# Kernel optimization log

Measured on AMD Instinct MI355X. Metric: run time of the kernel, lower is better.

Reference implementation:

```python
import jax, jax.numpy as jnp
import numpy as np

PI = jnp.pi

def phasor_encode(x):
    # map phase in [-1,1] to unit complex phasor exp(i*pi*x)
    return jnp.exp(jnp.complex64(1j) * PI * x.astype(jnp.float32))

def phasor_act(z):
    # angle of complex activation, normalized back to [-1,1]
    return jnp.angle(z) / PI

def multi_dense(x, w, b):
    # PhasorMultiDense: x [b,t,d], w [h,d,D], b [h,D] (complex bias, ones init)
    xz = phasor_encode(x)                                      # [b,t,d] complex64
    wz = w.astype(jnp.complex64)
    bz = b.astype(jnp.complex64)
    yz = jnp.einsum('btd,hdD->bhtD', xz, wz) + bz[None, :, None, :]
    return phasor_act(yz)                                      # [b,h,t,D] real

def attend(q, k, v):
    # VSA phasor attention: similarity = Re(qz . conj(kz)) / d, softmax, complex bundle of v phasors
    d = q.shape[-1]
    qz = phasor_encode(q)
    kz = phasor_encode(k)
    scores = jnp.real(jnp.einsum('bhtd,bhTd->bhtT', qz, jnp.conj(kz))) / d
    probs = jax.nn.softmax(scores, axis=-1)
    vz = phasor_encode(v)
    out = jnp.einsum('bhtT,bhTd->bhtd', probs.astype(jnp.complex64), vz)
    return phasor_act(out)                                     # [b,h,t,D]

def setup_inputs() -> dict:
    key = jax.random.key(0)
    ks = jax.random.split(key, 8)
    B, Tq, Tkv, D, H = 2, 1024, 1024, 512, 8
    sw = 1.0 / np.sqrt(D)       # VarianceScaling(1.0) fan_in
    swo = 1.0 / np.sqrt(H * D)
    return {
        'query': jax.random.uniform(ks[0], (B, Tq, D), jnp.float32, -1.0, 1.0),
        'keyvalue': jax.random.uniform(ks[1], (B, Tkv, D), jnp.float32, -1.0, 1.0),
        'wq': jax.random.normal(ks[2], (H, D, D), jnp.float32) * sw,
        'bq': jnp.ones((H, D), jnp.float32),
        'wk': jax.random.normal(ks[3], (H, D, D), jnp.float32) * sw,
        'bk': jnp.ones((H, D), jnp.float32),
        'wv': jax.random.normal(ks[4], (H, D, D), jnp.float32) * sw,
        'bv': jnp.ones((H, D), jnp.float32),
        'wo': jax.random.normal(ks[5], (H * D, D), jnp.float32) * swo,
        'bo': jnp.ones((D,), jnp.float32),
    }

def reference(query, keyvalue, wq, bq, wk, bk, wv, bv, wo, bo):
    q = multi_dense(query, wq, bq)        # [b,h,t,D]
    k = multi_dense(keyvalue, wk, bk)
    v = multi_dense(keyvalue, wv, bv)
    r = attend(q, k, v)                   # [b,h,t,D]
    b_, h_, t_, d_ = r.shape
    r_flat = jnp.transpose(r, (0, 2, 1, 3)).reshape(b_, t_, h_ * d_)  # b t (h d)
    # final PhasorDense
    xz = phasor_encode(r_flat)
    z = jnp.einsum('btd,dD->btD', xz, wo.astype(jnp.complex64)) + bo.astype(jnp.complex64)
    return phasor_act(z)                  # [b, t_q, output_channels]
```

## Files before the change

kernel.cpp:

```cpp
#include <hip/hip_runtime.h>
#include <math.h>


#define PI_F 3.14159274101257324f

typedef __attribute__((ext_vector_type(8))) _Float16 half8;
typedef __attribute__((ext_vector_type(4))) _Float16 half4;
typedef __attribute__((ext_vector_type(2))) _Float16 half2v;
typedef __attribute__((ext_vector_type(16))) float f32x16;
typedef unsigned int u32;

#define MFMA32(a, b, c) __builtin_amdgcn_mfma_f32_32x32x16_f16((a), (b), (c), 0, 0, 0)
#define ROWOF(r, ln) (((r) & 3) + 8 * ((r) >> 2) + 4 * ((ln) >> 5))

__device__ __forceinline__ void gll16(const void* g, void* l) {
    __builtin_amdgcn_global_load_lds(
        (const __attribute__((address_space(1))) u32*)g,
        (__attribute__((address_space(3))) u32*)l, 16, 0, 0);
}

__device__ __forceinline__ void split2(float x, _Float16& h, _Float16& l) {
    _Float16 hh = (_Float16)x;
    h = hh;
    l = (_Float16)((x - (float)hh) * 4096.0f);
}

__device__ __forceinline__ size_t feo(int m, int k, int Kd16) {
    return ((size_t)((m >> 5) * Kd16 + (k >> 4))) * 512
           + ((m & 31) + 32 * ((k >> 3) & 1)) * 8 + (k & 7);
}

__device__ __forceinline__ int xcdswz(int bid, int nwg) {
    const int cpx = nwg >> 3;
    return (bid & 7) * cpx + (bid >> 3);
}

__global__ __launch_bounds__(256) void encode_phasor(
    const float* __restrict__ x,
    _Float16* __restrict__ ch, _Float16* __restrict__ cl,
    _Float16* __restrict__ sh, _Float16* __restrict__ sl)
{
    const int idx = blockIdx.x * 256 + threadIdx.x;
    const int m = idx >> 7, k4 = (idx & 127) * 4;
    float4 v = ((const float4*)x)[idx];
    float cc[4], ss[4];
    sincosf(PI_F * v.x, &ss[0], &cc[0]);
    sincosf(PI_F * v.y, &ss[1], &cc[1]);
    sincosf(PI_F * v.z, &ss[2], &cc[2]);
    sincosf(PI_F * v.w, &ss[3], &cc[3]);
    half4 chv, clv, shv, slv;
#pragma unroll
    for (int q = 0; q < 4; ++q) {
        _Float16 a, b;
        split2(cc[q], a, b); chv[q] = a; clv[q] = b;
        split2(ss[q], a, b); shv[q] = a; slv[q] = b;
    }
    const size_t off = feo(m, k4, 32);
    *(half4*)(ch + off) = chv;
    *(half4*)(cl + off) = clv;
    *(half4*)(sh + off) = shv;
    *(half4*)(sl + off) = slv;
}

__global__ __launch_bounds__(256) void tsplit64(
    const float* __restrict__ w, _Float16* __restrict__ th, _Float16* __restrict__ tl,
    int K, int N)
{
    const int kt = blockIdx.x, ntile = blockIdx.y, h = blockIdx.z;
    const int k0 = kt * 64, n0 = ntile * 64;
    __shared__ float T[64][65];
    const int tid = threadIdx.x;
    const float* wb = w + (size_t)h * K * N;
    {
        const int r = tid >> 4, c4 = (tid & 15) * 4;
#pragma unroll
        for (int rr = 0; rr < 64; rr += 16) {
            float4 v = *(const float4*)&wb[(size_t)(k0 + rr + r) * N + n0 + c4];
            T[rr + r][c4 + 0] = v.x; T[rr + r][c4 + 1] = v.y;
            T[rr + r][c4 + 2] = v.z; T[rr + r][c4 + 3] = v.w;
        }
    }
    __syncthreads();
    {
        const int n = n0 + (tid >> 2), kq = k0 + (tid & 3) * 16;
        half8 hv[2], lv[2];
#pragma unroll
        for (int q = 0; q < 16; ++q) {
            float f = T[kq - k0 + q][n - n0];
            _Float16 hh, ll; split2(f, hh, ll);
            hv[q >> 3][q & 7] = hh; lv[q >> 3][q & 7] = ll;
        }
        const size_t hb = (size_t)h * 512 * K;
        const size_t offA = hb + ((size_t)((n >> 5) * (K >> 4) + (kq >> 4))) * 512
                            + (n & 31) * 8;
        *(half8*)(th + offA) = hv[0]; *(half8*)(th + offA + 256) = hv[1];
        *(half8*)(tl + offA) = lv[0]; *(half8*)(tl + offA + 256) = lv[1];
    }
}

template<bool VT>
__global__ __launch_bounds__(256, 2) void proj_mfma(
    const _Float16* __restrict__ xch, const _Float16* __restrict__ xcl,
    const _Float16* __restrict__ xsh, const _Float16* __restrict__ xsl,
    const _Float16* __restrict__ wth, const _Float16* __restrict__ wtl,
    const float* __restrict__ bias,
    _Float16* __restrict__ ozh, _Float16* __restrict__ ozl,
    _Float16* __restrict__ vc_h, _Float16* __restrict__ vc_l,
    _Float16* __restrict__ vs_h, _Float16* __restrict__ vs_l,
    int h0, int hcnt)
{
    const int m0 = blockIdx.x * 64;
    const int hc = blockIdx.y >> 2;
    const int n0 = (blockIdx.y & 3) * 128;
    __shared__ char lds[32768];
    const int tid = threadIdx.x, wv = tid >> 6, ln = tid & 63;
    const int wr = wv >> 1, wc = wv & 1, lm32 = ln & 31;

    const size_t abase = ((size_t)((m0 >> 5) + wr)) * 32 * 512 + ln * 8;
    const _Float16* pxc[2] = { xch + abase, xcl + abase };
    const _Float16* pxs[2] = { xsh + abase, xsl + abase };

    const char* spB[4]; int dpB[4];
#pragma unroll
    for (int u = 0; u < 4; ++u) {
        const int g = wv * 4 + u;
        const int jt = g >> 2, hl = (g >> 1) & 1, ks = g & 1;
        const _Float16* base = (hl ? wtl : wth) + (size_t)hc * 262144;
        spB[u] = (const char*)(base
                 + ((size_t)(((n0 + jt * 32) >> 5) * 32 + ks)) * 512 + ln * 8);
        dpB[u] = g * 1024;
    }

    f32x16 ach[2] = {}, acl[2] = {}, ash[2] = {}, asl[2] = {};

    auto LOADA = [&](int s, half8 (&ac)[2][2], half8 (&as)[2][2]) {
#pragma unroll
        for (int hl = 0; hl < 2; ++hl)
#pragma unroll
            for (int ks = 0; ks < 2; ++ks) {
                ac[hl][ks] = *(const half8*)(pxc[hl] + (2 * s + ks) * 512);
                as[hl][ks] = *(const half8*)(pxs[hl] + (2 * s + ks) * 512);
            }
    };
    auto STAGEB = [&](int s, int buf) {
#pragma unroll
        for (int u = 0; u < 4; ++u)
            gll16(spB[u] + (size_t)s * 2048, lds + buf + dpB[u]);
    };
    auto MSTEP = [&](int buf, half8 (&ac)[2][2], half8 (&as)[2][2]) {
        half8 w0[2][2], w1[2][2];
#pragma unroll
        for (int ks = 0; ks < 2; ++ks)
#pragma unroll
            for (int j = 0; j < 2; ++j) {
                const int gb = (wc * 2 + j) * 4 + ks;
                w0[ks][j] = *(const half8*)(lds + buf + gb * 1024 + ln * 16);
                w1[ks][j] = *(const half8*)(lds + buf + (gb + 2) * 1024 + ln * 16);
            }
        __builtin_amdgcn_s_setprio(1);
#pragma unroll
        for (int ks = 0; ks < 2; ++ks)
#pragma unroll
            for (int j = 0; j < 2; ++j) {
                ach[j] = MFMA32(ac[0][ks], w0[ks][j], ach[j]);
                acl[j] = MFMA32(ac[0][ks], w1[ks][j], acl[j]);
                acl[j] = MFMA32(ac[1][ks], w0[ks][j], acl[j]);
                ash[j] = MFMA32(as[0][ks], w0[ks][j], ash[j]);
                asl[j] = MFMA32(as[0][ks], w1[ks][j], asl[j]);
                asl[j] = MFMA32(as[1][ks], w0[ks][j], asl[j]);
            }
        __builtin_amdgcn_s_setprio(0);
    };

    half8 Ac0[2][2], As0[2][2], Ac1[2][2], As1[2][2];
    LOADA(0, Ac0, As0); STAGEB(0, 0);
    const int NS = 16;
    for (int s = 0; s < NS; s += 2) {
        __syncthreads();
        STAGEB(s + 1, 16384); LOADA(s + 1, Ac1, As1);
        MSTEP(0, Ac0, As0);
        __syncthreads();
        if (s + 2 < NS) { STAGEB(s + 2, 0); LOADA(s + 2, Ac0, As0); }
        MSTEP(16384, Ac1, As1);
    }

    const float LS = 1.0f / 4096.0f;
    const int b = m0 >> 10, tbase = m0 & 1023;
    const size_t zz = (size_t)(b * hcnt + hc);
    if constexpr (!VT) {
        const size_t zb = zz << 20;
#pragma unroll
        for (int j = 0; j < 2; ++j) {
            const int nloc = wc * 64 + j * 32 + lm32;
            const float bval = bias[(size_t)(h0 + hc) * 512 + n0 + nloc];
            const int kk = 2 * (n0 + nloc);
#pragma unroll
            for (int r = 0; r < 16; ++r) {
                const int mloc = wr * 32 + ROWOF(r, ln);
                float yc = ach[j][r] + acl[j][r] * LS + bval;
                float ys = ash[j][r] + asl[j][r] * LS;
                float inv = 1.0f / sqrtf(fmaxf(yc * yc + ys * ys, 1e-36f));
                float c = yc * inv, sn = ys * inv;
                _Float16 chh, chl, shh, shl;
                split2(c, chh, chl); split2(sn, shh, shl);
                const size_t off = zb + feo(tbase + mloc, kk, 64);
                half2v hv, lv;
                hv[0] = chh; hv[1] = shh; lv[0] = chl; lv[1] = shl;
                *(half2v*)(ozh + off) = hv;
                *(half2v*)(ozl + off) = lv;
            }
        }
    } else {
        _Float16 vh[4][2][16];
#pragma unroll
        for (int j = 0; j < 2; ++j) {
            const int nloc = wc * 64 + j * 32 + lm32;
            const float bval = bias[(size_t)(h0 + hc) * 512 + n0 + nloc];
#pragma unroll
            for (int r = 0; r < 16; ++r) {
                float yc = ach[j][r] + acl[j][r] * LS + bval;
                float ys = ash[j][r] + asl[j][r] * LS;
                float inv = 1.0f / sqrtf(fmaxf(yc * yc + ys * ys, 1e-36f));
                _Float16 a, bq_;
                split2(yc * inv, a, bq_); vh[0][j][r] = a; vh[1][j][r] = bq_;
                split2(ys * inv, a, bq_); vh[2][j][r] = a; vh[3][j][r] = bq_;
            }
        }
        const size_t zvb = zz * 524288;
        _Float16* outp[4] = { vc_h, vc_l, vs_h, vs_l };
#pragma unroll
        for (int p = 0; p < 4; ++p) {
            __syncthreads();
            _Float16* T = (_Float16*)lds;
#pragma unroll
            for (int j = 0; j < 2; ++j) {
                const int dloc = wc * 64 + j * 32 + lm32;
#pragma unroll
                for (int r = 0; r < 16; ++r)
                    T[dloc * 72 + wr * 32 + ROWOF(r, ln)] = vh[p][j][r];
            }
            __syncthreads();
            const int d_l = tid >> 1, seg = tid & 1;
            const int dg = n0 + d_l;
#pragma unroll
            for (int q = 0; q < 4; ++q) {
                const int tg = tbase + seg * 32 + q * 8;
                const size_t off = zvb + feo(dg, tg, 64);
                *(half8*)(outp[p] + off) = *(const half8*)(T + d_l * 72 + seg * 32 + q * 8);
            }
        }
    }
}

__global__ __launch_bounds__(256, 2) void scores_mfma(
    const _Float16* __restrict__ qzh, const _Float16* __restrict__ qzl,
    const _Float16* __restrict__ kzh, const _Float16* __restrict__ kzl,
    float* __restrict__ S, int Z)
{
    const int wg = xcdswz(blockIdx.x, Z * 64);
    const int z = wg >> 6;
    const int rem = wg & 63;
    const int m0 = (rem & 7) << 7, n0 = (rem >> 3) << 7;
    __shared__ char lds[32768];
    const size_t zb = (size_t)z << 20;
    const int tid = threadIdx.x, wv = tid >> 6, ln = tid & 63;
    const int wr = wv >> 1, wc = wv & 1, lm32 = ln & 31;

    const _Float16* pa[2] = { qzh + zb + ln * 8, qzl + zb + ln * 8 };
    const char* spB[4]; int dpB[4];
#pragma unroll
    for (int u = 0; u < 4; ++u) {
        const int g = wv * 4 + u;
        const int jt = g >> 2, hl = (g >> 1) & 1, ks = g & 1;
        spB[u] = (const char*)((hl ? kzl : kzh) + zb
                 + ((size_t)(((n0 + jt * 32) >> 5) * 64 + ks)) * 512 + ln * 8);
        dpB[u] = g * 1024;
    }

    f32x16 acch[2][2] = {}, accl[2][2] = {};

    auto LOADA = [&](int s, half8 (&a)[2][2][2]) {
#pragma unroll
        for (int hl = 0; hl < 2; ++hl)
#pragma unroll
            for (int i = 0; i < 2; ++i)
#pragma unroll
                for (int ks = 0; ks < 2; ++ks)
                    a[hl][i][ks] = *(const half8*)(pa[hl]
                        + ((size_t)((m0 >> 5) + wr * 2 + i) * 64 + 2 * s + ks) * 512);
    };
    auto STAGEB = [&](int s, int buf) {
#pragma unroll
        for (int u = 0; u < 4; ++u)
            gll16(spB[u] + (size_t)s * 2048, lds + buf + dpB[u]);
    };
    auto MSTEP = [&](int buf, half8 (&a)[2][2][2]) {
        half8 bh[2][2], bl[2][2];
#pragma unroll
        for (int ks = 0; ks < 2; ++ks)
#pragma unroll
            for (int j = 0; j < 2; ++j) {
                const int gb = (wc * 2 + j) * 4 + ks;
                bh[ks][j] = *(const half8*)(lds + buf + gb * 1024 + ln * 16);
                bl[ks][j] = *(const half8*)(lds + buf + (gb + 2) * 1024 + ln * 16);
            }
        __builtin_amdgcn_s_setprio(1);
#pragma unroll
        for (int ks = 0; ks < 2; ++ks)
#pragma unroll
            for (int i = 0; i < 2; ++i)
#pragma unroll
                for (int j = 0; j < 2; ++j) {
                    acch[i][j] = MFMA32(a[0][i][ks], bh[ks][j], acch[i][j]);
                    accl[i][j] = MFMA32(a[0][i][ks], bl[ks][j], accl[i][j]);
                    accl[i][j] = MFMA32(a[1][i][ks], bh[ks][j], accl[i][j]);
                }
        __builtin_amdgcn_s_setprio(0);
    };

    half8 A0[2][2][2], A1[2][2][2];
    LOADA(0, A0); STAGEB(0, 0);
    const int NS = 32;
    for (int s = 0; s < NS; s += 2) {
        __syncthreads();
        STAGEB(s + 1, 16384); LOADA(s + 1, A1);
        MSTEP(0, A0);
        __syncthreads();
        if (s + 2 < NS) { STAGEB(s + 2, 0); LOADA(s + 2, A0); }
        MSTEP(16384, A1);
    }
    const float LS = 1.0f / 4096.0f, SC = 1.0f / 512.0f;
#pragma unroll
    for (int i = 0; i < 2; ++i)
#pragma unroll
        for (int j = 0; j < 2; ++j)
#pragma unroll
            for (int r = 0; r < 16; ++r) {
                const int row = m0 + wr * 64 + i * 32 + ROWOF(r, ln);
                const int col = n0 + wc * 64 + j * 32 + lm32;
                S[zb + (size_t)row * 1024 + col] =
                    (acch[i][j][r] + accl[i][j][r] * LS) * SC;
            }
}

__global__ __launch_bounds__(256) void softmax_split(
    const float* __restrict__ S, _Float16* __restrict__ Ph, _Float16* __restrict__ Pl)
{
    const int z = blockIdx.x >> 10, t = blockIdx.x & 1023;
    const float* p = S + ((size_t)blockIdx.x << 10);
    const int tid = threadIdx.x;
    float4 v = ((const float4*)p)[tid];
    float m = fmaxf(fmaxf(v.x, v.y), fmaxf(v.z, v.w));
#pragma unroll
    for (int off = 32; off >= 1; off >>= 1)
        m = fmaxf(m, __shfl_xor(m, off));
    __shared__ float redm[4], reds[4];
    const int wid = tid >> 6, lane = tid & 63;
    if (lane == 0) redm[wid] = m;
    __syncthreads();
    m = fmaxf(fmaxf(redm[0], redm[1]), fmaxf(redm[2], redm[3]));
    float4 e;
    e.x = expf(v.x - m); e.y = expf(v.y - m);
    e.z = expf(v.z - m); e.w = expf(v.w - m);
    float s = (e.x + e.y) + (e.z + e.w);
#pragma unroll
    for (int off = 32; off >= 1; off >>= 1)
        s += __shfl_xor(s, off);
    if (lane == 0) reds[wid] = s;
    __syncthreads();
    s = (reds[0] + reds[1]) + (reds[2] + reds[3]);
    e.x /= s; e.y /= s; e.z /= s; e.w /= s;
    half4 hv, lv;
    _Float16 a, b;
    split2(e.x, a, b); hv[0] = a; lv[0] = b;
    split2(e.y, a, b); hv[1] = a; lv[1] = b;
    split2(e.z, a, b); hv[2] = a; lv[2] = b;
    split2(e.w, a, b); hv[3] = a; lv[3] = b;
    const size_t off = ((size_t)z << 20) + feo(t, tid * 4, 64);
    *(half4*)(Ph + off) = hv;
    *(half4*)(Pl + off) = lv;
}

__global__ __launch_bounds__(256, 2) void pv_mfma(
    const _Float16* __restrict__ Ph, const _Float16* __restrict__ Pl,
    const _Float16* __restrict__ vch, const _Float16* __restrict__ vcl,
    const _Float16* __restrict__ vsh, const _Float16* __restrict__ vsl,
    _Float16* __restrict__ rch, _Float16* __restrict__ rcl,
    _Float16* __restrict__ rsh, _Float16* __restrict__ rsl,
    int h0, int hcnt, int Z)
{
    const int wg = xcdswz(blockIdx.x, Z * 64);
    const int z = wg >> 6;
    const int rem = wg & 63;
    const int m0 = (rem & 7) << 7, n0 = (rem >> 3) << 6;
    __shared__ char lds[32768];
    const int tid = threadIdx.x, wv = tid >> 6, ln = tid & 63;
    const int wr = wv >> 1, wc = wv & 1, lm32 = ln & 31;

    const size_t zb = (size_t)z << 20, zvb = (size_t)z * 524288;
    const _Float16* pa[2] = { Ph + zb + ln * 8, Pl + zb + ln * 8 };
    const char* spB[4]; int dpB[4];
#pragma unroll
    for (int u = 0; u < 4; ++u) {
        const int g = wv * 4 + u;
        const int pl = g >> 3, dt = (g >> 2) & 1, hl = (g >> 1) & 1, ks = g & 1;
        const _Float16* base = pl ? (hl ? vsl : vsh) : (hl ? vcl : vch);
        spB[u] = (const char*)(base + zvb
                 + ((size_t)(((n0 + dt * 32) >> 5) * 64 + ks)) * 512 + ln * 8);
        dpB[u] = g * 1024;
    }

    f32x16 ac_h[2] = {}, ac_l[2] = {}, as_h[2] = {}, as_l[2] = {};

    auto LOADA = [&](int s, half8 (&a)[2][2][2]) {
#pragma unroll
        for (int hl = 0; hl < 2; ++hl)
#pragma unroll
            for (int i = 0; i < 2; ++i)
#pragma unroll
                for (int ks = 0; ks < 2; ++ks)
                    a[hl][i][ks] = *(const half8*)(pa[hl]
                        + ((size_t)((m0 >> 5) + wr * 2 + i) * 64 + 2 * s + ks) * 512);
    };
    auto STAGEB = [&](int s, int buf) {
#pragma unroll
        for (int u = 0; u < 4; ++u)
            gll16(spB[u] + (size_t)s * 2048, lds + buf + dpB[u]);
    };
    auto MSTEP = [&](int buf, half8 (&a)[2][2][2]) {
        half8 vc[2][2], vs[2][2];
#pragma unroll
        for (int hl = 0; hl < 2; ++hl)
#pragma unroll
            for (int ks = 0; ks < 2; ++ks) {
                vc[hl][ks] = *(const half8*)(lds + buf + (wc * 4 + hl * 2 + ks) * 1024 + ln * 16);
                vs[hl][ks] = *(const half8*)(lds + buf + (8 + wc * 4 + hl * 2 + ks) * 1024 + ln * 16);
            }
        __builtin_amdgcn_s_setprio(1);
#pragma unroll
        for (int ks = 0; ks < 2; ++ks)
#pragma unroll
            for (int i = 0; i < 2; ++i) {
                ac_h[i] = MFMA32(a[0][i][ks], vc[0][ks], ac_h[i]);
                ac_l[i] = MFMA32(a[0][i][ks], vc[1][ks], ac_l[i]);
                ac_l[i] = MFMA32(a[1][i][ks], vc[0][ks], ac_l[i]);
                as_h[i] = MFMA32(a[0][i][ks], vs[0][ks], as_h[i]);
                as_l[i] = MFMA32(a[0][i][ks], vs[1][ks], as_l[i]);
                as_l[i] = MFMA32(a[1][i][ks], vs[0][ks], as_l[i]);
            }
        __builtin_amdgcn_s_setprio(0);
    };

    half8 A0[2][2][2], A1[2][2][2];
    LOADA(0, A0); STAGEB(0, 0);
    const int NS = 32;
    for (int s = 0; s < NS; s += 2) {
        __syncthreads();
        STAGEB(s + 1, 16384); LOADA(s + 1, A1);
        MSTEP(0, A0);
        __syncthreads();
        if (s + 2 < NS) { STAGEB(s + 2, 0); LOADA(s + 2, A0); }
        MSTEP(16384, A1);
    }
    const float LS = 1.0f / 4096.0f;
    const int b = z / hcnt, hg = h0 + z % hcnt;
#pragma unroll
    for (int i = 0; i < 2; ++i)
#pragma unroll
        for (int r = 0; r < 16; ++r) {
            const int t = m0 + wr * 64 + i * 32 + ROWOF(r, ln);
            const int d = n0 + wc * 32 + lm32;
            float zc = ac_h[i][r] + ac_l[i][r] * LS;
            float zs = as_h[i][r] + as_l[i][r] * LS;
            float inv = 1.0f / sqrtf(fmaxf(zc * zc + zs * zs, 1e-36f));
            _Float16 chh, chl, shh, shl;
            split2(zc * inv, chh, chl);
            split2(zs * inv, shh, shl);
            const size_t off = feo(b * 1024 + t, hg * 512 + d, 256);
            rch[off] = chh; rcl[off] = chl; rsh[off] = shh; rsl[off] = shl;
        }
}

__global__ __launch_bounds__(256, 2) void final_mfma(
    const _Float16* __restrict__ rch, const _Float16* __restrict__ rcl,
    const _Float16* __restrict__ rsh, const _Float16* __restrict__ rsl,
    const _Float16* __restrict__ woh, const _Float16* __restrict__ wol,
    float* __restrict__ pbuf)
{
    const int m0 = blockIdx.x * 64, n0 = blockIdx.y * 128;
    const int kspl = blockIdx.z;
    const int kf = kspl * 64;
    __shared__ char lds[32768];
    const int tid = threadIdx.x, wv = tid >> 6, ln = tid & 63;
    const int wr = wv >> 1, wc = wv & 1, lm32 = ln & 31;

    const size_t abase = ((size_t)((m0 >> 5) + wr) * 256 + kf) * 512 + ln * 8;
    const _Float16* prc[2] = { rch + abase, rcl + abase };
    const _Float16* prs[2] = { rsh + abase, rsl + abase };
    const char* spB[4]; int dpB[4];
#pragma unroll
    for (int u = 0; u < 4; ++u) {
        const int g = wv * 4 + u;
        const int jt = g >> 2, hl = (g >> 1) & 1, ks = g & 1;
        spB[u] = (const char*)((hl ? wol : woh)
                 + ((size_t)(((n0 + jt * 32) >> 5) * 256 + kf + ks)) * 512 + ln * 8);
        dpB[u] = g * 1024;
    }

    f32x16 rr_h[2] = {}, rr_l[2] = {}, ri_h[2] = {}, ri_l[2] = {};

    auto LOADA = [&](int s, half8 (&ac)[2][2], half8 (&as)[2][2]) {
#pragma unroll
        for (int hl = 0; hl < 2; ++hl)
#pragma unroll
            for (int ks = 0; ks < 2; ++ks) {
                ac[hl][ks] = *(const half8*)(prc[hl] + (2 * s + ks) * 512);
                as[hl][ks] = *(const half8*)(prs[hl] + (2 * s + ks) * 512);
            }
    };
    auto STAGEB = [&](int s, int buf) {
#pragma unroll
        for (int u = 0; u < 4; ++u)
            gll16(spB[u] + (size_t)s * 2048, lds + buf + dpB[u]);
    };
    auto MSTEP = [&](int buf, half8 (&ac)[2][2], half8 (&as)[2][2]) {
        half8 w0[2][2], w1[2][2];
#pragma unroll
        for (int ks = 0; ks < 2; ++ks)
#pragma unroll
            for (int j = 0; j < 2; ++j) {
                const int gb = (wc * 2 + j) * 4 + ks;
                w0[ks][j] = *(const half8*)(lds + buf + gb * 1024 + ln * 16);
                w1[ks][j] = *(const half8*)(lds + buf + (gb + 2) * 1024 + ln * 16);
            }
        __builtin_amdgcn_s_setprio(1);
#pragma unroll
        for (int ks = 0; ks < 2; ++ks)
#pragma unroll
            for (int j = 0; j < 2; ++j) {
                rr_h[j] = MFMA32(ac[0][ks], w0[ks][j], rr_h[j]);
                rr_l[j] = MFMA32(ac[0][ks], w1[ks][j], rr_l[j]);
                rr_l[j] = MFMA32(ac[1][ks], w0[ks][j], rr_l[j]);
                ri_h[j] = MFMA32(as[0][ks], w0[ks][j], ri_h[j]);
                ri_l[j] = MFMA32(as[0][ks], w1[ks][j], ri_l[j]);
                ri_l[j] = MFMA32(as[1][ks], w0[ks][j], ri_l[j]);
            }
        __builtin_amdgcn_s_setprio(0);
    };

    half8 Ac0[2][2], As0[2][2], Ac1[2][2], As1[2][2];
    LOADA(0, Ac0, As0); STAGEB(0, 0);
    const int NS = 32;
    for (int s = 0; s < NS; s += 2) {
        __syncthreads();
        STAGEB(s + 1, 16384); LOADA(s + 1, Ac1, As1);
        MSTEP(0, Ac0, As0);
        __syncthreads();
        if (s + 2 < NS) { STAGEB(s + 2, 0); LOADA(s + 2, Ac0, As0); }
        MSTEP(16384, Ac1, As1);
    }
    const float LS = 1.0f / 4096.0f;
#pragma unroll
    for (int j = 0; j < 2; ++j) {
        const int ng = n0 + wc * 64 + j * 32 + lm32;
#pragma unroll
        for (int r = 0; r < 16; ++r) {
            const int mg = m0 + wr * 32 + ROWOF(r, ln);
            float2 v;
            v.x = rr_h[j][r] + rr_l[j][r] * LS;
            v.y = ri_h[j][r] + ri_l[j][r] * LS;
            *(float2*)&pbuf[((size_t)(kspl * 2048 + mg) * 512 + ng) * 2] = v;
        }
    }
}

__global__ __launch_bounds__(256) void final_combine(
    const float* __restrict__ pbuf, const float* __restrict__ bo,
    float* __restrict__ out, int KS)
{
    const int m = blockIdx.x, t = threadIdx.x;
    float4 acc = {0.f, 0.f, 0.f, 0.f};
    for (int s = 0; s < KS; ++s) {
        float4 v = *(const float4*)&pbuf[(size_t)(s * 2048 + m) * 1024 + t * 4];
        acc.x += v.x; acc.y += v.y; acc.z += v.z; acc.w += v.w;
    }
    const int n0 = t * 2;
    out[(size_t)m * 512 + n0]     = atan2f(acc.y, acc.x + bo[n0]) / PI_F;
    out[(size_t)m * 512 + n0 + 1] = atan2f(acc.w, acc.z + bo[n0 + 1]) / PI_F;
}

extern "C" void kernel_launch(void* const* d_in, const int* in_sizes, int n_in,
                              void* d_out, int out_size, void* d_ws, size_t ws_size,
                              hipStream_t stream)
{
    (void)in_sizes; (void)n_in; (void)out_size;
    const float* query    = (const float*)d_in[0];
    const float* keyvalue = (const float*)d_in[1];
    const float* wq = (const float*)d_in[2];
    const float* bq = (const float*)d_in[3];
    const float* wk = (const float*)d_in[4];
    const float* bk = (const float*)d_in[5];
    const float* wv = (const float*)d_in[6];
    const float* bv = (const float*)d_in[7];
    const float* wo = (const float*)d_in[8];
    const float* bo = (const float*)d_in[9];
    float* out = (float*)d_out;

    int hcnt;
    if (ws_size >= (size_t)320 * 1024 * 1024) hcnt = 8;
    else if (ws_size >= (size_t)240 * 1024 * 1024) hcnt = 4;
    else hcnt = 2;
    const int Z = 2 * hcnt;
    const int KS = (hcnt == 2) ? 2 : 4;

    char* p = (char*)d_ws;
    auto alloc = [&](size_t bytes) {
        char* r = p;
        p += (bytes + 255) & ~(size_t)255;
        return r;
    };
    const size_t PLX = (size_t)2048 * 512;
    _Float16* xq[4]; for (int i = 0; i < 4; ++i) xq[i] = (_Float16*)alloc(PLX * 2);
    _Float16* xk[4]; for (int i = 0; i < 4; ++i) xk[i] = (_Float16*)alloc(PLX * 2);
    _Float16* woT[2]; for (int i = 0; i < 2; ++i) woT[i] = (_Float16*)alloc((size_t)512 * 4096 * 2);
    const size_t WTE = (size_t)hcnt * 512 * 512;
    _Float16* wqT[2]; for (int i = 0; i < 2; ++i) wqT[i] = (_Float16*)alloc(WTE * 2);
    _Float16* wkT[2]; for (int i = 0; i < 2; ++i) wkT[i] = (_Float16*)alloc(WTE * 2);
    _Float16* wvT[2]; for (int i = 0; i < 2; ++i) wvT[i] = (_Float16*)alloc(WTE * 2);
    const size_t QZE = (size_t)Z * 1024 * 1024;
    _Float16* qz[2]; for (int i = 0; i < 2; ++i) qz[i] = (_Float16*)alloc(QZE * 2);
    _Float16* kz[2]; for (int i = 0; i < 2; ++i) kz[i] = (_Float16*)alloc(QZE * 2);
    float* S = (float*)alloc(QZE * 4);
    const size_t VTE = (size_t)Z * 512 * 1024;
    _Float16* vT[4]; for (int i = 0; i < 4; ++i) vT[i] = (_Float16*)alloc(VTE * 2);
    const size_t RCE = (size_t)2048 * 4096;
    _Float16* rcs[4];
    if (hcnt == 8) {
        for (int i = 0; i < 4; ++i) rcs[i] = (_Float16*)((char*)qz[0] + (size_t)i * RCE * 2);
    } else {
        for (int i = 0; i < 4; ++i) rcs[i] = (_Float16*)alloc(RCE * 2);
    }
    _Float16* Ph = kz[0];
    _Float16* Pl = kz[1];
    float* pbuf = (float*)kz[0];

    dim3 blk(256);

    encode_phasor<<<1024, blk, 0, stream>>>(query, xq[0], xq[1], xq[2], xq[3]);
    encode_phasor<<<1024, blk, 0, stream>>>(keyvalue, xk[0], xk[1], xk[2], xk[3]);
    tsplit64<<<dim3(64, 8, 1), blk, 0, stream>>>(wo, woT[0], woT[1], 4096, 512);

    for (int c = 0; c < 8 / hcnt; ++c) {
        const int h0 = c * hcnt;
        const float* wqc = wq + (size_t)h0 * 512 * 512;
        const float* wkc = wk + (size_t)h0 * 512 * 512;
        const float* wvc = wv + (size_t)h0 * 512 * 512;
        tsplit64<<<dim3(8, 8, hcnt), blk, 0, stream>>>(wqc, wqT[0], wqT[1], 512, 512);
        tsplit64<<<dim3(8, 8, hcnt), blk, 0, stream>>>(wkc, wkT[0], wkT[1], 512, 512);
        tsplit64<<<dim3(8, 8, hcnt), blk, 0, stream>>>(wvc, wvT[0], wvT[1], 512, 512);

        proj_mfma<false><<<dim3(32, hcnt * 4), blk, 0, stream>>>(
            xq[0], xq[1], xq[2], xq[3], wqT[0], wqT[1], bq,
            qz[0], qz[1], nullptr, nullptr, nullptr, nullptr, h0, hcnt);
        proj_mfma<false><<<dim3(32, hcnt * 4), blk, 0, stream>>>(
            xk[0], xk[1], xk[2], xk[3], wkT[0], wkT[1], bk,
            kz[0], kz[1], nullptr, nullptr, nullptr, nullptr, h0, hcnt);
        proj_mfma<true><<<dim3(32, hcnt * 4), blk, 0, stream>>>(
            xk[0], xk[1], xk[2], xk[3], wvT[0], wvT[1], bv,
            nullptr, nullptr, vT[0], vT[1], vT[2], vT[3], h0, hcnt);

        scores_mfma<<<dim3(Z * 64), blk, 0, stream>>>(qz[0], qz[1], kz[0], kz[1], S, Z);
        softmax_split<<<dim3(Z * 1024), blk, 0, stream>>>(S, Ph, Pl);
        pv_mfma<<<dim3(Z * 64), blk, 0, stream>>>(
            Ph, Pl, vT[0], vT[1], vT[2], vT[3],
            rcs[0], rcs[1], rcs[2], rcs[3], h0, hcnt, Z);
    }

    final_mfma<<<dim3(32, 4, KS), blk, 0, stream>>>(
        rcs[0], rcs[1], rcs[2], rcs[3], woT[0], woT[1], pbuf);
    final_combine<<<dim3(2048), blk, 0, stream>>>(pbuf, bo, out, KS);
}
```

Baseline: 595.4 us.

## Stage fragment-layout outputs through LDS and merge encode/split/projection launches

Epilogues in encode, projection, softmax and PV kernels now stage results in LDS and write full 16-byte fragment-layout chunks, replacing scattered 2-byte and 4-byte global stores. Encode, weight-split and Q/K projection launches are merged into fewer kernels via grid z-dimension selection. Softmax is restructured to process 32 rows per block and drops the max subtraction, since scores are bounded by 1 in magnitude. These changes aim to cut store-transaction overhead and launch count, at the cost of extra LDS round trips and barriers.

```diff
diff --git a/kernel.cpp b/kernel.cpp
--- a/kernel.cpp
+++ b/kernel.cpp
@@ -25,41 +25,64 @@
     l = (_Float16)((x - (float)hh) * 4096.0f);
 }
 
-__device__ __forceinline__ size_t feo(int m, int k, int Kd16) {
-    return ((size_t)((m >> 5) * Kd16 + (k >> 4))) * 512
-           + ((m & 31) + 32 * ((k >> 3) & 1)) * 8 + (k & 7);
-}
-
 __device__ __forceinline__ int xcdswz(int bid, int nwg) {
     const int cpx = nwg >> 3;
     return (bid & 7) * cpx + (bid >> 3);
 }
 
 __global__ __launch_bounds__(256) void encode_phasor(
-    const float* __restrict__ x,
-    _Float16* __restrict__ ch, _Float16* __restrict__ cl,
-    _Float16* __restrict__ sh, _Float16* __restrict__ sl)
-{
-    const int idx = blockIdx.x * 256 + threadIdx.x;
-    const int m = idx >> 7, k4 = (idx & 127) * 4;
-    float4 v = ((const float4*)x)[idx];
-    float cc[4], ss[4];
-    sincosf(PI_F * v.x, &ss[0], &cc[0]);
-    sincosf(PI_F * v.y, &ss[1], &cc[1]);
-    sincosf(PI_F * v.z, &ss[2], &cc[2]);
-    sincosf(PI_F * v.w, &ss[3], &cc[3]);
-    half4 chv, clv, shv, slv;
-#pragma unroll
-    for (int q = 0; q < 4; ++q) {
-        _Float16 a, b;
-        split2(cc[q], a, b); chv[q] = a; clv[q] = b;
-        split2(ss[q], a, b); shv[q] = a; slv[q] = b;
-    }
-    const size_t off = feo(m, k4, 32);
-    *(half4*)(ch + off) = chv;
-    *(half4*)(cl + off) = clv;
-    *(half4*)(sh + off) = shv;
-    *(half4*)(sl + off) = slv;
+    const float* __restrict__ xq, const float* __restrict__ xkv,
+    _Float16* __restrict__ qch, _Float16* __restrict__ qcl,
+    _Float16* __restrict__ qsh, _Float16* __restrict__ qsl,
+    _Float16* __restrict__ kch, _Float16* __restrict__ kcl,
+    _Float16* __restrict__ ksh, _Float16* __restrict__ ksl)
+{
+    const int mt = blockIdx.x, yh = blockIdx.y, zi = blockIdx.z;
+    const float* x = zi ? xkv : xq;
+    __shared__ char fb[32768];
+    const int tid = threadIdx.x;
+    const int row = tid >> 3, lc = tid & 7;
+    const float* xr = x + (size_t)(mt * 32 + row) * 512 + yh * 256;
+    for (int c = 0; c < 2; ++c) {
+        if (c) __syncthreads();
+        half8 hs[4][2];
+#pragma unroll
+        for (int g = 0; g < 2; ++g)
+#pragma unroll
+            for (int q = 0; q < 2; ++q) {
+                float4 v = *(const float4*)(xr + c * 128 + lc * 16 + g * 8 + q * 4);
+                float cc[4], ss[4];
+                sincosf(PI_F * v.x, &ss[0], &cc[0]);
+                sincosf(PI_F * v.y, &ss[1], &cc[1]);
+                sincosf(PI_F * v.z, &ss[2], &cc[2]);
+                sincosf(PI_F * v.w, &ss[3], &cc[3]);
+#pragma unroll
+                for (int e = 0; e < 4; ++e) {
+                    _Float16 a, b;
+                    split2(cc[e], a, b); hs[0][g][q * 4 + e] = a; hs[1][g][q * 4 + e] = b;
+                    split2(ss[e], a, b); hs[2][g][q * 4 + e] = a; hs[3][g][q * 4 + e] = b;
+                }
+            }
+#pragma unroll
+        for (int p = 0; p < 4; ++p) {
+            char* base = fb + p * 8192 + lc * 1024 + row * 16;
+            *(half8*)(base) = hs[p][0];
+            *(half8*)(base + 512) = hs[p][1];
+        }
+        __syncthreads();
+#pragma unroll
+        for (int w = 0; w < 8; ++w) {
+            const int u = w * 256 + tid;
+            const int p = u >> 9, rest = u & 511;
+            const int f = rest >> 6, within = rest & 63;
+            _Float16* op;
+            if (zi) op = (p == 0) ? kch : (p == 1) ? kcl : (p == 2) ? ksh : ksl;
+            else    op = (p == 0) ? qch : (p == 1) ? qcl : (p == 2) ? qsh : qsl;
+            const size_t fragG = (size_t)mt * 32 + yh * 16 + c * 8 + f;
+            *(half8*)(op + fragG * 512 + within * 8) =
+                *(const half8*)(fb + p * 8192 + f * 1024 + within * 16);
+        }
+    }
 }
 
 __global__ __launch_bounds__(256) void tsplit64(
@@ -98,17 +121,71 @@
     }
 }
 
-template<bool VT>
-__global__ __launch_bounds__(256, 2) void proj_mfma(
-    const _Float16* __restrict__ xch, const _Float16* __restrict__ xcl,
-    const _Float16* __restrict__ xsh, const _Float16* __restrict__ xsl,
-    const _Float16* __restrict__ wth, const _Float16* __restrict__ wtl,
-    const float* __restrict__ bias,
-    _Float16* __restrict__ ozh, _Float16* __restrict__ ozl,
-    _Float16* __restrict__ vc_h, _Float16* __restrict__ vc_l,
-    _Float16* __restrict__ vs_h, _Float16* __restrict__ vs_l,
+__global__ __launch_bounds__(256) void tsplit_qkv(
+    const float* __restrict__ wq, const float* __restrict__ wk,
+    const float* __restrict__ wv,
+    _Float16* __restrict__ qh, _Float16* __restrict__ ql,
+    _Float16* __restrict__ kh, _Float16* __restrict__ kl,
+    _Float16* __restrict__ vh, _Float16* __restrict__ vl, int hcnt)
+{
+    const int tsel = blockIdx.z / hcnt, h = blockIdx.z % hcnt;
+    const int kt = blockIdx.x, ntile = blockIdx.y;
+    const int k0 = kt * 64, n0 = ntile * 64;
+    const float* w = (tsel == 0) ? wq : (tsel == 1) ? wk : wv;
+    _Float16* th = (tsel == 0) ? qh : (tsel == 1) ? kh : vh;
+    _Float16* tl = (tsel == 0) ? ql : (tsel == 1) ? kl : vl;
+    __shared__ float T[64][65];
+    const int tid = threadIdx.x;
+    const float* wb = w + (size_t)h * 262144;
+    {
+        const int r = tid >> 4, c4 = (tid & 15) * 4;
+#pragma unroll
+        for (int rr = 0; rr < 64; rr += 16) {
+            float4 v = *(const float4*)&wb[(size_t)(k0 + rr + r) * 512 + n0 + c4];
+            T[rr + r][c4 + 0] = v.x; T[rr + r][c4 + 1] = v.y;
+            T[rr + r][c4 + 2] = v.z; T[rr + r][c4 + 3] = v.w;
+        }
+    }
+    __syncthreads();
+    {
+        const int n = n0 + (tid >> 2), kq = k0 + (tid & 3) * 16;
+        half8 hv[2], lv[2];
+#pragma unroll
+        for (int q = 0; q < 16; ++q) {
+            float f = T[kq - k0 + q][n - n0];
+            _Float16 hh, ll; split2(f, hh, ll);
+            hv[q >> 3][q & 7] = hh; lv[q >> 3][q & 7] = ll;
+        }
+        const size_t hb = (size_t)h * 262144;
+        const size_t offA = hb + ((size_t)((n >> 5) * 32 + (kq >> 4))) * 512 + (n & 31) * 8;
+        *(half8*)(th + offA) = hv[0]; *(half8*)(th + offA + 256) = hv[1];
+        *(half8*)(tl + offA) = lv[0]; *(half8*)(tl + offA + 256) = lv[1];
+    }
+}
+
+__global__ __launch_bounds__(256, 2) void proj_qk(
+    const _Float16* __restrict__ qch, const _Float16* __restrict__ qcl,
+    const _Float16* __restrict__ qsh, const _Float16* __restrict__ qsl,
+    const _Float16* __restrict__ kch, const _Float16* __restrict__ kcl,
+    const _Float16* __restrict__ ksh, const _Float16* __restrict__ ksl,
+    const _Float16* __restrict__ wqh, const _Float16* __restrict__ wql,
+    const _Float16* __restrict__ wkh, const _Float16* __restrict__ wkl,
+    const float* __restrict__ bq, const float* __restrict__ bk,
+    _Float16* __restrict__ qzh, _Float16* __restrict__ qzl,
+    _Float16* __restrict__ kzh, _Float16* __restrict__ kzl,
     int h0, int hcnt)
 {
+    const int inp = blockIdx.z;
+    const _Float16* xch = inp ? kch : qch;
+    const _Float16* xcl = inp ? kcl : qcl;
+    const _Float16* xsh = inp ? ksh : qsh;
+    const _Float16* xsl = inp ? ksl : qsl;
+    const _Float16* wth = inp ? wkh : wqh;
+    const _Float16* wtl = inp ? wkl : wql;
+    const float* bias = inp ? bk : bq;
+    _Float16* ozh = inp ? kzh : qzh;
+    _Float16* ozl = inp ? kzl : qzl;
+
     const int m0 = blockIdx.x * 64;
     const int hc = blockIdx.y >> 2;
     const int n0 = (blockIdx.y & 3) * 128;
@@ -187,67 +264,165 @@
     const float LS = 1.0f / 4096.0f;
     const int b = m0 >> 10, tbase = m0 & 1023;
     const size_t zz = (size_t)(b * hcnt + hc);
-    if constexpr (!VT) {
-        const size_t zb = zz << 20;
+    const size_t zb = zz << 20;
+    __syncthreads();
+#pragma unroll
+    for (int p = 0; p < 2; ++p) {
+        if (p) __syncthreads();
 #pragma unroll
         for (int j = 0; j < 2; ++j) {
             const int nloc = wc * 64 + j * 32 + lm32;
             const float bval = bias[(size_t)(h0 + hc) * 512 + n0 + nloc];
-            const int kk = 2 * (n0 + nloc);
+            const int kk = 2 * nloc;
 #pragma unroll
             for (int r = 0; r < 16; ++r) {
                 const int mloc = wr * 32 + ROWOF(r, ln);
                 float yc = ach[j][r] + acl[j][r] * LS + bval;
                 float ys = ash[j][r] + asl[j][r] * LS;
                 float inv = 1.0f / sqrtf(fmaxf(yc * yc + ys * ys, 1e-36f));
-                float c = yc * inv, sn = ys * inv;
-                _Float16 chh, chl, shh, shl;
-                split2(c, chh, chl); split2(sn, shh, shl);
-                const size_t off = zb + feo(tbase + mloc, kk, 64);
-                half2v hv, lv;
-                hv[0] = chh; hv[1] = shh; lv[0] = chl; lv[1] = shl;
-                *(half2v*)(ozh + off) = hv;
-                *(half2v*)(ozl + off) = lv;
-            }
-        }
-    } else {
-        _Float16 vh[4][2][16];
+                _Float16 c_h, c_l, s_h, s_l;
+                split2(yc * inv, c_h, c_l);
+                split2(ys * inv, s_h, s_l);
+                half2v pr;
+                pr[0] = p ? c_l : c_h;
+                pr[1] = p ? s_l : s_h;
+                *(half2v*)(lds + ((mloc >> 5) * 16 + (kk >> 4)) * 1024
+                    + (mloc & 31) * 16 + 512 * ((kk >> 3) & 1) + (kk & 7) * 2) = pr;
+            }
+        }
+        __syncthreads();
+        _Float16* op = p ? ozl : ozh;
+#pragma unroll
+        for (int w = 0; w < 8; ++w) {
+            const int u = w * 256 + tid;
+            const int f = u >> 6, within = u & 63;
+            const int ms = f >> 4, kf = f & 15;
+            *(half8*)(op + zb + (((size_t)(tbase >> 5) + ms) * 64 + (n0 >> 3) + kf) * 512
+                      + within * 8) = *(const half8*)(lds + f * 1024 + within * 16);
+        }
+    }
+}
+
+__global__ __launch_bounds__(256, 2) void proj_v(
+    const _Float16* __restrict__ xch, const _Float16* __restrict__ xcl,
+    const _Float16* __restrict__ xsh, const _Float16* __restrict__ xsl,
+    const _Float16* __restrict__ wth, const _Float16* __restrict__ wtl,
+    const float* __restrict__ bias,
+    _Float16* __restrict__ vc_h, _Float16* __restrict__ vc_l,
+    _Float16* __restrict__ vs_h, _Float16* __restrict__ vs_l,
+    int h0, int hcnt)
+{
+    const int m0 = blockIdx.x * 64;
+    const int hc = blockIdx.y >> 2;
+    const int n0 = (blockIdx.y & 3) * 128;
+    __shared__ char lds[32768];
+    const int tid = threadIdx.x, wv = tid >> 6, ln = tid & 63;
+    const int wr = wv >> 1, wc = wv & 1, lm32 = ln & 31;
+
+    const size_t abase = ((size_t)((m0 >> 5) + wr)) * 32 * 512 + ln * 8;
+    const _Float16* pxc[2] = { xch + abase, xcl + abase };
+    const _Float16* pxs[2] = { xsh + abase, xsl + abase };
+
+    const char* spB[4]; int dpB[4];
+#pragma unroll
+    for (int u = 0; u < 4; ++u) {
+        const int g = wv * 4 + u;
+        const int jt = g >> 2, hl = (g >> 1) & 1, ks = g & 1;
+        const _Float16* base = (hl ? wtl : wth) + (size_t)hc * 262144;
+        spB[u] = (const char*)(base
+                 + ((size_t)(((n0 + jt * 32) >> 5) * 32 + ks)) * 512 + ln * 8);
+        dpB[u] = g * 1024;
+    }
+
+    f32x16 ach[2] = {}, acl[2] = {}, ash[2] = {}, asl[2] = {};
+
+    auto LOADA = [&](int s, half8 (&ac)[2][2], half8 (&as)[2][2]) {
+#pragma unroll
+        for (int hl = 0; hl < 2; ++hl)
+#pragma unroll
+            for (int ks = 0; ks < 2; ++ks) {
+                ac[hl][ks] = *(const half8*)(pxc[hl] + (2 * s + ks) * 512);
+                as[hl][ks] = *(const half8*)(pxs[hl] + (2 * s + ks) * 512);
+            }
+    };
+    auto STAGEB = [&](int s, int buf) {
+#pragma unroll
+        for (int u = 0; u < 4; ++u)
+            gll16(spB[u] + (size_t)s * 2048, lds + buf + dpB[u]);
+    };
+    auto MSTEP = [&](int buf, half8 (&ac)[2][2], half8 (&as)[2][2]) {
+        half8 w0[2][2], w1[2][2];
+#pragma unroll
+        for (int ks = 0; ks < 2; ++ks)
+#pragma unroll
+            for (int j = 0; j < 2; ++j) {
+                const int gb = (wc * 2 + j) * 4 + ks;
+                w0[ks][j] = *(const half8*)(lds + buf + gb * 1024 + ln * 16);
+                w1[ks][j] = *(const half8*)(lds + buf + (gb + 2) * 1024 + ln * 16);
+            }
+        __builtin_amdgcn_s_setprio(1);
+#pragma unroll
+        for (int ks = 0; ks < 2; ++ks)
+#pragma unroll
+            for (int j = 0; j < 2; ++j) {
+                ach[j] = MFMA32(ac[0][ks], w0[ks][j], ach[j]);
+                acl[j] = MFMA32(ac[0][ks], w1[ks][j], acl[j]);
+                acl[j] = MFMA32(ac[1][ks], w0[ks][j], acl[j]);
+                ash[j] = MFMA32(as[0][ks], w0[ks][j], ash[j]);
+                asl[j] = MFMA32(as[0][ks], w1[ks][j], asl[j]);
+                asl[j] = MFMA32(as[1][ks], w0[ks][j], asl[j]);
+            }
+        __builtin_amdgcn_s_setprio(0);
+    };
+
+    half8 Ac0[2][2], As0[2][2], Ac1[2][2], As1[2][2];
+    LOADA(0, Ac0, As0); STAGEB(0, 0);
+    const int NS = 16;
+    for (int s = 0; s < NS; s += 2) {
+        __syncthreads();
+        STAGEB(s + 1, 16384); LOADA(s + 1, Ac1, As1);
+        MSTEP(0, Ac0, As0);
+        __syncthreads();
+        if (s + 2 < NS) { STAGEB(s + 2, 0); LOADA(s + 2, Ac0, As0); }
+        MSTEP(16384, Ac1, As1);
+    }
+
+    const float LS = 1.0f / 4096.0f;
+    const int b = m0 >> 10, tbase = m0 & 1023;
+    const size_t zz = (size_t)(b * hcnt + hc);
+    const size_t zvb = zz * 524288;
+    _Float16* T = (_Float16*)lds;
+#pragma unroll
+    for (int p = 0; p < 4; ++p) {
+        __syncthreads();
 #pragma unroll
         for (int j = 0; j < 2; ++j) {
-            const int nloc = wc * 64 + j * 32 + lm32;
-            const float bval = bias[(size_t)(h0 + hc) * 512 + n0 + nloc];
+            const int dloc = wc * 64 + j * 32 + lm32;
+            const float bval = bias[(size_t)(h0 + hc) * 512 + n0 + dloc];
 #pragma unroll
             for (int r = 0; r < 16; ++r) {
+                const int tloc = wr * 32 + ROWOF(r, ln);
                 float yc = ach[j][r] + acl[j][r] * LS + bval;
                 float ys = ash[j][r] + asl[j][r] * LS;
                 float inv = 1.0f / sqrtf(fmaxf(yc * yc + ys * ys, 1e-36f));
-                _Float16 a, bq_;
-                split2(yc * inv, a, bq_); vh[0][j][r] = a; vh[1][j][r] = bq_;
-                split2(ys * inv, a, bq_); vh[2][j][r] = a; vh[3][j][r] = bq_;
-            }
-        }
-        const size_t zvb = zz * 524288;
-        _Float16* outp[4] = { vc_h, vc_l, vs_h, vs_l };
-#pragma unroll
-        for (int p = 0; p < 4; ++p) {
-            __syncthreads();
-            _Float16* T = (_Float16*)lds;
-#pragma unroll
-            for (int j = 0; j < 2; ++j) {
-                const int dloc = wc * 64 + j * 32 + lm32;
-#pragma unroll
-                for (int r = 0; r < 16; ++r)
-                    T[dloc * 72 + wr * 32 + ROWOF(r, ln)] = vh[p][j][r];
-            }
-            __syncthreads();
-            const int d_l = tid >> 1, seg = tid & 1;
-            const int dg = n0 + d_l;
-#pragma unroll
-            for (int q = 0; q < 4; ++q) {
-                const int tg = tbase + seg * 32 + q * 8;
-                const size_t off = zvb + feo(dg, tg, 64);
-                *(half8*)(outp[p] + off) = *(const half8*)(T + d_l * 72 + seg * 32 + q * 8);
-            }
+                _Float16 hh, ll;
+                if (p < 2) split2(yc * inv, hh, ll);
+                else       split2(ys * inv, hh, ll);
+                T[dloc * 80 + tloc] = (p & 1) ? ll : hh;
+            }
+        }
+        __syncthreads();
+        _Float16* op = (p == 0) ? vc_h : (p == 1) ? vc_l : (p == 2) ? vs_h : vs_l;
+#pragma unroll
+        for (int w = 0; w < 4; ++w) {
+            const int u = w * 256 + tid;
+            const int f = u >> 6, within = u & 63;
+            const int ds_ = f >> 2, tf = f & 3;
+            const int d = ds_ * 32 + (within & 31);
+            const int tl = tf * 16 + (within >> 5) * 8;
+            half8 vv = *(const half8*)(T + d * 80 + tl);
+            *(half8*)(op + zvb + (((size_t)((n0 >> 5) + ds_)) * 64 + (tbase >> 4) + tf) * 512
+                      + within * 8) = vv;
         }
     }
 }
@@ -343,42 +518,52 @@
             }
 }
 
-__global__ __launch_bounds__(256) void softmax_split(
+__global__ __launch_bounds__(256) void softmax_frag(
     const float* __restrict__ S, _Float16* __restrict__ Ph, _Float16* __restrict__ Pl)
 {
-    const int z = blockIdx.x >> 10, t = blockIdx.x & 1023;
-    const float* p = S + ((size_t)blockIdx.x << 10);
+    const int z = blockIdx.x >> 5, tt = blockIdx.x & 31;
+    const float* Sb = S + ((size_t)z << 20) + ((size_t)tt << 15);
     const int tid = threadIdx.x;
-    float4 v = ((const float4*)p)[tid];
-    float m = fmaxf(fmaxf(v.x, v.y), fmaxf(v.z, v.w));
-#pragma unroll
-    for (int off = 32; off >= 1; off >>= 1)
-        m = fmaxf(m, __shfl_xor(m, off));
-    __shared__ float redm[4], reds[4];
-    const int wid = tid >> 6, lane = tid & 63;
-    if (lane == 0) redm[wid] = m;
+    const int row = tid >> 3, lc = tid & 7;
+    __shared__ float rsum[32];
+    __shared__ char fb[32768];
+    const float* prow = Sb + (size_t)row * 1024 + lc * 128;
+    float s = 0.f;
+    for (int q = 0; q < 32; ++q) {
+        float4 v = *(const float4*)(prow + q * 4);
+        s += (expf(v.x) + expf(v.y)) + (expf(v.z) + expf(v.w));
+    }
+    s += __shfl_xor(s, 1); s += __shfl_xor(s, 2); s += __shfl_xor(s, 4);
+    if (lc == 0) rsum[row] = s;
     __syncthreads();
-    m = fmaxf(fmaxf(redm[0], redm[1]), fmaxf(redm[2], redm[3]));
-    float4 e;
-    e.x = expf(v.x - m); e.y = expf(v.y - m);
-    e.z = expf(v.z - m); e.w = expf(v.w - m);
-    float s = (e.x + e.y) + (e.z + e.w);
-#pragma unroll
-    for (int off = 32; off >= 1; off >>= 1)
-        s += __shfl_xor(s, off);
-    if (lane == 0) reds[wid] = s;
-    __syncthreads();
-    s = (reds[0] + reds[1]) + (reds[2] + reds[3]);
-    e.x /= s; e.y /= s; e.z /= s; e.w /= s;
-    half4 hv, lv;
-    _Float16 a, b;
-    split2(e.x, a, b); hv[0] = a; lv[0] = b;
-    split2(e.y, a, b); hv[1] = a; lv[1] = b;
-    split2(e.z, a, b); hv[2] = a; lv[2] = b;
-    split2(e.w, a, b); hv[3] = a; lv[3] = b;
-    const size_t off = ((size_t)z << 20) + feo(t, tid * 4, 64);
-    *(half4*)(Ph + off) = hv;
-    *(half4*)(Pl + off) = lv;
+    const float inv = 1.0f / rsum[row];
+    for (int c = 0; c < 4; ++c) {
+        if (c) __syncthreads();
+        const float* pc = Sb + (size_t)row * 1024 + c * 256 + lc * 32;
+#pragma unroll
+        for (int q = 0; q < 8; ++q) {
+            float4 v = *(const float4*)(pc + q * 4);
+            half4 hv, lv; _Float16 a, b;
+            split2(expf(v.x) * inv, a, b); hv[0] = a; lv[0] = b;
+            split2(expf(v.y) * inv, a, b); hv[1] = a; lv[1] = b;
+            split2(expf(v.z) * inv, a, b); hv[2] = a; lv[2] = b;
+            split2(expf(v.w) * inv, a, b); hv[3] = a; lv[3] = b;
+            const int f = lc * 2 + (q >> 2);
+            const int boff = f * 1024 + row * 16 + 512 * ((q >> 1) & 1) + (q & 1) * 8;
+            *(half4*)(fb + boff) = hv;
+            *(half4*)(fb + 16384 + boff) = lv;
+        }
+        __syncthreads();
+#pragma unroll
+        for (int w = 0; w < 8; ++w) {
+            const int u = w * 256 + tid;
+            const int pl = u >> 10, rest = u & 1023;
+            const int f = rest >> 6, within = rest & 63;
+            _Float16* dst = (pl ? Pl : Ph) + ((size_t)z << 20)
+                          + ((size_t)(tt * 64 + c * 16 + f)) * 512 + within * 8;
+            *(half8*)dst = *(const half8*)(fb + pl * 16384 + f * 1024 + within * 16);
+        }
+    }
 }
 
 __global__ __launch_bounds__(256, 2) void pv_mfma(
@@ -464,21 +649,39 @@
     }
     const float LS = 1.0f / 4096.0f;
     const int b = z / hcnt, hg = h0 + z % hcnt;
-#pragma unroll
-    for (int i = 0; i < 2; ++i)
-#pragma unroll
-        for (int r = 0; r < 16; ++r) {
-            const int t = m0 + wr * 64 + i * 32 + ROWOF(r, ln);
-            const int d = n0 + wc * 32 + lm32;
-            float zc = ac_h[i][r] + ac_l[i][r] * LS;
-            float zs = as_h[i][r] + as_l[i][r] * LS;
-            float inv = 1.0f / sqrtf(fmaxf(zc * zc + zs * zs, 1e-36f));
-            _Float16 chh, chl, shh, shl;
-            split2(zc * inv, chh, chl);
-            split2(zs * inv, shh, shl);
-            const size_t off = feo(b * 1024 + t, hg * 512 + d, 256);
-            rch[off] = chh; rcl[off] = chl; rsh[off] = shh; rsl[off] = shl;
-        }
+    const size_t mrow = (size_t)((b * 1024 + m0) >> 5);
+    const size_t kcol = (size_t)(hg * 512 + n0) >> 4;
+    __syncthreads();
+#pragma unroll
+    for (int p = 0; p < 4; ++p) {
+        if (p) __syncthreads();
+#pragma unroll
+        for (int i = 0; i < 2; ++i)
+#pragma unroll
+            for (int r = 0; r < 16; ++r) {
+                const int mloc = wr * 64 + i * 32 + ROWOF(r, ln);
+                const int kloc = wc * 32 + lm32;
+                float zc = ac_h[i][r] + ac_l[i][r] * LS;
+                float zs = as_h[i][r] + as_l[i][r] * LS;
+                float inv = 1.0f / sqrtf(fmaxf(zc * zc + zs * zs, 1e-36f));
+                _Float16 hh, ll;
+                if (p < 2) split2(zc * inv, hh, ll);
+                else       split2(zs * inv, hh, ll);
+                *(_Float16*)(lds + ((mloc >> 5) * 4 + (kloc >> 4)) * 1024
+                    + (mloc & 31) * 16 + 512 * ((kloc >> 3) & 1) + (kloc & 7) * 2)
+                    = (p & 1) ? ll : hh;
+            }
+        __syncthreads();
+        _Float16* op = (p == 0) ? rch : (p == 1) ? rcl : (p == 2) ? rsh : rsl;
+#pragma unroll
+        for (int w = 0; w < 4; ++w) {
+            const int u = w * 256 + tid;
+            const int f = u >> 6, within = u & 63;
+            const int ms = f >> 2, kf = f & 3;
+            *(half8*)(op + ((mrow + ms) * 256 + kcol + kf) * 512 + within * 8)
+                = *(const half8*)(lds + f * 1024 + within * 16);
+        }
+    }
 }
 
 __global__ __launch_bounds__(256, 2) void final_mfma(
@@ -646,31 +849,27 @@
 
     dim3 blk(256);
 
-    encode_phasor<<<1024, blk, 0, stream>>>(query, xq[0], xq[1], xq[2], xq[3]);
-    encode_phasor<<<1024, blk, 0, stream>>>(keyvalue, xk[0], xk[1], xk[2], xk[3]);
+    encode_phasor<<<dim3(64, 2, 2), blk, 0, stream>>>(
+        query, keyvalue,
+        xq[0], xq[1], xq[2], xq[3], xk[0], xk[1], xk[2], xk[3]);
     tsplit64<<<dim3(64, 8, 1), blk, 0, stream>>>(wo, woT[0], woT[1], 4096, 512);
 
     for (int c = 0; c < 8 / hcnt; ++c) {
         const int h0 = c * hcnt;
-        const float* wqc = wq + (size_t)h0 * 512 * 512;
-        const float* wkc = wk + (size_t)h0 * 512 * 512;
-        const float* wvc = wv + (size_t)h0 * 512 * 512;
-        tsplit64<<<dim3(8, 8, hcnt), blk, 0, stream>>>(wqc, wqT[0], wqT[1], 512, 512);
-        tsplit64<<<dim3(8, 8, hcnt), blk, 0, stream>>>(wkc, wkT[0], wkT[1], 512, 512);
-        tsplit64<<<dim3(8, 8, hcnt), blk, 0, stream>>>(wvc, wvT[0], wvT[1], 512, 512);
-
-        proj_mfma<false><<<dim3(32, hcnt * 4), blk, 0, stream>>>(
-            xq[0], xq[1], xq[2], xq[3], wqT[0], wqT[1], bq,
-            qz[0], qz[1], nullptr, nullptr, nullptr, nullptr, h0, hcnt);
-        proj_mfma<false><<<dim3(32, hcnt * 4), blk, 0, stream>>>(
-            xk[0], xk[1], xk[2], xk[3], wkT[0], wkT[1], bk,
-            kz[0], kz[1], nullptr, nullptr, nullptr, nullptr, h0, hcnt);
-        proj_mfma<true><<<dim3(32, hcnt * 4), blk, 0, stream>>>(
+        tsplit_qkv<<<dim3(8, 8, 3 * hcnt), blk, 0, stream>>>(
+            wq + (size_t)h0 * 262144, wk + (size_t)h0 * 262144, wv + (size_t)h0 * 262144,
+            wqT[0], wqT[1], wkT[0], wkT[1], wvT[0], wvT[1], hcnt);
+
+        proj_qk<<<dim3(32, hcnt * 4, 2), blk, 0, stream>>>(
+            xq[0], xq[1], xq[2], xq[3], xk[0], xk[1], xk[2], xk[3],
+            wqT[0], wqT[1], wkT[0], wkT[1], bq, bk,
+            qz[0], qz[1], kz[0], kz[1], h0, hcnt);
+        proj_v<<<dim3(32, hcnt * 4), blk, 0, stream>>>(
             xk[0], xk[1], xk[2], xk[3], wvT[0], wvT[1], bv,
-            nullptr, nullptr, vT[0], vT[1], vT[2], vT[3], h0, hcnt);
+            vT[0], vT[1], vT[2], vT[3], h0, hcnt);
 
         scores_mfma<<<dim3(Z * 64), blk, 0, stream>>>(qz[0], qz[1], kz[0], kz[1], S, Z);
-        softmax_split<<<dim3(Z * 1024), blk, 0, stream>>>(S, Ph, Pl);
+        softmax_frag<<<dim3(Z * 32), blk, 0, stream>>>(S, Ph, Pl);
         pv_mfma<<<dim3(Z * 64), blk, 0, stream>>>(
             Ph, Pl, vT[0], vT[1], vT[2], vT[3],
             rcs[0], rcs[1], rcs[2], rcs[3], h0, hcnt, Z);
```

After: 587.1 us. Within noise of the previous version (-1.4%).
